# Kernel optimization log

Measured on AMD Instinct MI355X. Metric: run time of the kernel, lower is better.

The kernel has to match this reference:

```python
import jax, jax.numpy as jnp
import numpy as np

B, T, D, H = 4096, 512, 25, 25
NUM_LAYERS = 3


def setup_inputs() -> dict:
    key = jax.random.key(0)
    ks = jax.random.split(key, 9)
    s = 1.0 / np.sqrt(H)  # torch LSTM/Linear default init scale
    return {
        "x": jax.random.normal(ks[0], (B, T, D), dtype=jnp.float32),
        "Wih": jax.random.uniform(ks[1], (NUM_LAYERS, 4 * H, D), minval=-s, maxval=s),
        "Whh": jax.random.uniform(ks[2], (NUM_LAYERS, 4 * H, H), minval=-s, maxval=s),
        "bih": jax.random.uniform(ks[3], (NUM_LAYERS, 4 * H), minval=-s, maxval=s),
        "bhh": jax.random.uniform(ks[4], (NUM_LAYERS, 4 * H), minval=-s, maxval=s),
        "W1": jax.random.uniform(ks[5], (16, H), minval=-s, maxval=s),
        "b1": jax.random.uniform(ks[6], (16,), minval=-s, maxval=s),
        "W2": jax.random.uniform(ks[7], (14, 16), minval=-0.25, maxval=0.25),
        "b2": jax.random.uniform(ks[8], (14,), minval=-0.25, maxval=0.25),
    }


def _lstm_layer(x, Wih, Whh, b):
    """Single LSTM layer, batch_first. x: [B,T,Din] -> hs: [B,T,H].
    Torch gate order: i, f, g, o."""
    # Precompute input contribution for all timesteps at once: [B,T,4H]
    xg = jnp.einsum('btd,gd->btg', x, Wih) + b

    def step(carry, xg_t):
        h, c = carry
        g = xg_t + h @ Whh.T  # [B,4H]
        i, f, gg, o = jnp.split(g, 4, axis=-1)
        c = jax.nn.sigmoid(f) * c + jax.nn.sigmoid(i) * jnp.tanh(gg)
        h = jax.nn.sigmoid(o) * jnp.tanh(c)
        return (h, c), h

    h0 = jnp.zeros((x.shape[0], H), x.dtype)
    (_, _), hs = jax.lax.scan(step, (h0, h0), jnp.swapaxes(xg, 0, 1))  # [T,B,H]
    return jnp.swapaxes(hs, 0, 1)


def reference(x, Wih, Whh, bih, bhh, W1, b1, W2, b2):
    h = x
    for l in range(NUM_LAYERS):  # eval mode: inter-layer dropout disabled
        h = _lstm_layer(h, Wih[l], Whh[l], bih[l] + bhh[l])
    last = h[:, -1, :]                       # [B,H]
    out = jax.nn.relu(last @ W1.T + b1)      # [B,16]
    return jax.nn.softmax(out @ W2.T + b2, axis=1)  # [B,14]
```

## Files before the change

### kernel.cpp

```cpp
#include <hip/hip_runtime.h>


#define NBATCH 4096
#define NT     512
#define ND     25
#define NG     100
#define NL     3

__device__ __forceinline__ float sigf(float x) {
    return __builtin_amdgcn_rcpf(1.0f + __expf(-x));
}
__device__ __forceinline__ float tanhfast(float x) {
    float s = sigf(x + x);
    return s + s - 1.0f;
}

__global__ __launch_bounds__(256, 4)
void lstm2(const float* __restrict__ xin,
           const float* __restrict__ Wih,
           const float* __restrict__ Whh,
           const float* __restrict__ bih,
           const float* __restrict__ bhh,
           const float* __restrict__ W1,
           const float* __restrict__ b1,
           const float* __restrict__ W2,
           const float* __restrict__ b2,
           float* __restrict__ out,
           float* __restrict__ ws)
{
    __shared__ __align__(16) float xh[2][56];
    __shared__ float act[2][112];

    const int wid  = threadIdx.x >> 6;
    const int lane = threadIdx.x & 63;
    const int wb   = wid >> 1;
    const int role = wid & 1;
    const int b    = (blockIdx.x << 1) + wb;

    const int  lrow    = (lane < 50) ? lane : 49;
    const bool updater = (role == 0) && (lane < 25);

    float w[52];
    w[50] = 0.f; w[51] = 0.f;

    for (int l = 0; l < NL; ++l) {
        const int row = l * NG + role * 50 + lrow;
        const float* wihp = Wih + row * ND;
        const float* whhp = Whh + row * ND;
#pragma unroll
        for (int d = 0; d < 25; ++d) { w[d] = wihp[d]; w[25 + d] = whhp[d]; }
        const float bias = bih[row] + bhh[row];

        const float* src = (l == 0) ? (xin + (size_t)b * NT * ND)
                                    : (ws  + (size_t)b * NT * ND);
        float* wsrow = ws + (size_t)b * NT * ND;

        float c = 0.f;
        float xv_next = 0.f;
        if (updater) {
            xh[wb][lane] = src[lane];
            xv_next = src[ND + lane];
        }
        if (role == 0 && lane < 31) xh[wb][25 + lane] = 0.f;
        __syncthreads();

        for (int t = 0; t < NT; ++t) {
            float acc = bias;
#pragma unroll
            for (int c4 = 0; c4 < 13; ++c4) {
                const float4 v = *(const float4*)&xh[wb][c4 * 4];
                acc = fmaf(w[c4 * 4 + 0], v.x, acc);
                acc = fmaf(w[c4 * 4 + 1], v.y, acc);
                acc = fmaf(w[c4 * 4 + 2], v.z, acc);
                acc = fmaf(w[c4 * 4 + 3], v.w, acc);
            }
            float a;
            if (role == 0) a = sigf(acc);
            else           a = (lane < 25) ? tanhfast(acc)
                                           : sigf(acc);
            if (lane < 50) act[wb][role * 56 + lane] = a;
            __syncthreads();

            if (updater) {
                const float ig = act[wb][lane];
                const float fg = act[wb][25 + lane];
                const float gg = act[wb][56 + lane];
                const float og = act[wb][81 + lane];
                c = fmaf(fg, c, ig * gg);
                const float h = og * tanhfast(c);
                xh[wb][25 + lane] = h;
                xh[wb][lane]      = xv_next;
                if (l < 2) wsrow[t * ND + lane] = h;
                if (t + 2 < NT) xv_next = src[(t + 2) * ND + lane];
            }
            __syncthreads();
        }
    }

    if (role == 0 && lane < 16) {
        float u = b1[lane];
#pragma unroll
        for (int d = 0; d < 25; ++d) u = fmaf(W1[lane * 25 + d], xh[wb][25 + d], u);
        act[wb][lane] = fmaxf(u, 0.f);
    }
    if (role == 0 && lane < 14) {
        float lg = b2[lane];
#pragma unroll
        for (int r = 0; r < 16; ++r) lg = fmaf(W2[lane * 16 + r], act[wb][r], lg);
        act[wb][32 + lane] = lg;
    }
    if (role == 0 && lane < 14) {
        float m = -1e30f;
#pragma unroll
        for (int j = 0; j < 14; ++j) m = fmaxf(m, act[wb][32 + j]);
        float sum = 0.f;
#pragma unroll
        for (int j = 0; j < 14; ++j) sum += __expf(act[wb][32 + j] - m);
        out[b * 14 + lane] = __expf(act[wb][32 + lane] - m) / sum;
    }
}

extern "C" void kernel_launch(void* const* d_in, const int* in_sizes, int n_in,
                              void* d_out, int out_size, void* d_ws, size_t ws_size,
                              hipStream_t stream)
{
    const float* x   = (const float*)d_in[0];
    const float* Wih = (const float*)d_in[1];
    const float* Whh = (const float*)d_in[2];
    const float* bih = (const float*)d_in[3];
    const float* bhh = (const float*)d_in[4];
    const float* W1  = (const float*)d_in[5];
    const float* b1  = (const float*)d_in[6];
    const float* W2  = (const float*)d_in[7];
    const float* b2  = (const float*)d_in[8];
    float* outp = (float*)d_out;
    float* ws   = (float*)d_ws;

    dim3 grid(NBATCH / 2), block(256);
    hipLaunchKernelGGL(lstm2, grid, block, 0, stream,
                       x, Wih, Whh, bih, bhh, W1, b1, W2, b2, outp, ws);
}
```

Measured before the change: 1.884 ms.

## Rewrite LSTM recurrence as single-wave MFMA kernel with split-fp16 precision

Replaces the per-batch scalar FMA kernel, which used four waves per block with block-wide barriers each timestep, with one 64-thread wave per 16 batch rows. Gate pre-activations are computed with 16x16x32 fp16 MFMAs, using a hi/lo split of weights and inputs to approximate fp32 accuracy, and the bias is folded in through a constant-1 column. Each lane updates gates for its own rows in registers, so no workgroup barriers are needed, and inter-layer activations are stored as packed fp16 hi/lo pairs. The grid shrinks to 256 single-wave blocks, which may underuse the GPU's CUs, and the split-precision arithmetic introduces small numerical error.

```diff
diff --git a/kernel.cpp b/kernel.cpp
--- a/kernel.cpp
+++ b/kernel.cpp
@@ -1,22 +1,28 @@
 #include <hip/hip_runtime.h>
-
-
-#define NBATCH 4096
-#define NT     512
-#define ND     25
-#define NG     100
-#define NL     3
-
-__device__ __forceinline__ float sigf(float x) {
-    return __builtin_amdgcn_rcpf(1.0f + __expf(-x));
-}
-__device__ __forceinline__ float tanhfast(float x) {
-    float s = sigf(x + x);
-    return s + s - 1.0f;
-}
-
-__global__ __launch_bounds__(256, 4)
-void lstm2(const float* __restrict__ xin,
+#include <cstdint>
+
+
+typedef _Float16 f16;
+typedef f16  f16x8 __attribute__((ext_vector_type(8)));
+typedef float f32x4 __attribute__((ext_vector_type(4)));
+
+#define NT 512
+#define ND 25
+#define LOSCALE 4096.0f
+#define INVLO   2.44140625e-4f
+
+__device__ __forceinline__ float exp2f_(float x){ return __builtin_amdgcn_exp2f(x); }
+__device__ __forceinline__ float rcpf_(float x){ return __builtin_amdgcn_rcpf(x); }
+__device__ __forceinline__ float sigf(float x){ return rcpf_(1.f + exp2f_(-1.442695041f*x)); }
+__device__ __forceinline__ float tanhf_(float x){ return fmaf(2.f, rcpf_(1.f + exp2f_(-2.885390082f*x)), -1.f); }
+
+__device__ __forceinline__ unsigned short f16b(f16 h){ union{f16 h; unsigned short s;} u; u.h=h; return u.s; }
+__device__ __forceinline__ f16 b2f16(unsigned short s){ union{f16 h; unsigned short s;} u; u.s=s; return u.h; }
+
+#define MFMA(a,b,c) __builtin_amdgcn_mfma_f32_16x16x32_f16((a),(b),(c),0,0,0)
+
+__global__ __launch_bounds__(64, 1)
+void lstm9(const float* __restrict__ xin,
            const float* __restrict__ Wih,
            const float* __restrict__ Whh,
            const float* __restrict__ bih,
@@ -26,97 +32,206 @@
            const float* __restrict__ W2,
            const float* __restrict__ b2,
            float* __restrict__ out,
-           float* __restrict__ ws)
+           uint32_t* __restrict__ ws)
 {
-    __shared__ __align__(16) float xh[2][56];
-    __shared__ float act[2][112];
-
-    const int wid  = threadIdx.x >> 6;
-    const int lane = threadIdx.x & 63;
-    const int wb   = wid >> 1;
-    const int role = wid & 1;
-    const int b    = (blockIdx.x << 1) + wb;
-
-    const int  lrow    = (lane < 50) ? lane : 49;
-    const bool updater = (role == 0) && (lane < 25);
-
-    float w[52];
-    w[50] = 0.f; w[51] = 0.f;
-
-    for (int l = 0; l < NL; ++l) {
-        const int row = l * NG + role * 50 + lrow;
-        const float* wihp = Wih + row * ND;
-        const float* whhp = Whh + row * ND;
-#pragma unroll
-        for (int d = 0; d < 25; ++d) { w[d] = wihp[d]; w[25 + d] = whhp[d]; }
-        const float bias = bih[row] + bhh[row];
-
-        const float* src = (l == 0) ? (xin + (size_t)b * NT * ND)
-                                    : (ws  + (size_t)b * NT * ND);
-        float* wsrow = ws + (size_t)b * NT * ND;
-
-        float c = 0.f;
-        float xv_next = 0.f;
-        if (updater) {
-            xh[wb][lane] = src[lane];
-            xv_next = src[ND + lane];
-        }
-        if (role == 0 && lane < 31) xh[wb][25 + lane] = 0.f;
-        __syncthreads();
+    __shared__ __align__(16) f16 WH[14*64*8];
+    __shared__ __align__(16) f16 WL[14*64*8];
+    __shared__ __align__(16) f16 XH_H[16*72];
+    __shared__ __align__(16) f16 XH_L[16*72];
+    __shared__ __align__(16) float hfin[16*28];
+
+    const int L  = threadIdx.x;
+    const int bq = L & 15;
+    const int lg = L >> 4;
+    const int bb = blockIdx.x * 16;
+
+    for (int i = L; i < 16*72; i += 64) { XH_H[i] = (f16)0.f; XH_L[i] = (f16)0.f; }
+    if (L < 16) XH_H[L*72 + 63] = (f16)1.f;
+
+    float c0,c1,c2,c3,c4,c5,c6;
+    float h0=0,h1=0,h2=0,h3=0,h4=0,h5=0,h6=0;
+
+    for (int l = 0; l < 3; ++l) {
+        asm volatile("s_waitcnt vmcnt(0)" ::: "memory");
+
+        for (int blk = 0; blk < 14; ++blk) {
+            const int mt = blk >> 1, kt = blk & 1;
+            const int rp = mt*16 + bq;
+            const int u  = rp >> 2, g = rp & 3;
+            const int ro = g*25 + u;
+            f16x8 vh, vl;
+#pragma unroll
+            for (int i = 0; i < 8; ++i) {
+                const int k = kt*32 + lg*8 + i;
+                float w = 0.f;
+                if (rp < 100) {
+                    if (k < 25)       w = Wih[((size_t)l*100 + ro)*25 + k];
+                    else if (k < 50)  w = Whh[((size_t)l*100 + ro)*25 + (k-25)];
+                    else if (k == 63) w = bih[l*100 + ro] + bhh[l*100 + ro];
+                }
+                const f16 hi = (f16)w;
+                vh[i] = hi;
+                vl[i] = (f16)((w - (float)hi) * LOSCALE);
+            }
+            *(f16x8*)&WH[blk*512 + L*8] = vh;
+            *(f16x8*)&WL[blk*512 + L*8] = vl;
+        }
+
+        const bool isl0 = (l == 0);
+        const float*    srcx = xin + (size_t)(bb)*NT*ND;
+        const uint32_t* srcw = ws  + (size_t)(bb)*NT*ND;
+
+        c0=c1=c2=c3=c4=c5=c6=0.f;
+#pragma unroll
+        for (int j = 0; j < 7; ++j) {
+            const int u = lg + 4*j;
+            if (u < 25) {
+                XH_H[bq*72 + 25 + u] = (f16)0.f;
+                XH_L[bq*72 + 25 + u] = (f16)0.f;
+                f16 hi, lo;
+                if (isl0) {
+                    const float v = srcx[((size_t)bq*NT + 0)*ND + u];
+                    hi = (f16)v; lo = (f16)((v - (float)hi) * LOSCALE);
+                } else {
+                    const uint32_t p = srcw[((size_t)bq*NT + 0)*ND + u];
+                    hi = b2f16((unsigned short)(p & 0xffff));
+                    lo = b2f16((unsigned short)(p >> 16));
+                }
+                XH_H[bq*72 + u] = hi;
+                XH_L[bq*72 + u] = lo;
+            }
+        }
 
         for (int t = 0; t < NT; ++t) {
-            float acc = bias;
-#pragma unroll
-            for (int c4 = 0; c4 < 13; ++c4) {
-                const float4 v = *(const float4*)&xh[wb][c4 * 4];
-                acc = fmaf(w[c4 * 4 + 0], v.x, acc);
-                acc = fmaf(w[c4 * 4 + 1], v.y, acc);
-                acc = fmaf(w[c4 * 4 + 2], v.z, acc);
-                acc = fmaf(w[c4 * 4 + 3], v.w, acc);
-            }
-            float a;
-            if (role == 0) a = sigf(acc);
-            else           a = (lane < 25) ? tanhfast(acc)
-                                           : sigf(acc);
-            if (lane < 50) act[wb][role * 56 + lane] = a;
-            __syncthreads();
-
-            if (updater) {
-                const float ig = act[wb][lane];
-                const float fg = act[wb][25 + lane];
-                const float gg = act[wb][56 + lane];
-                const float og = act[wb][81 + lane];
-                c = fmaf(fg, c, ig * gg);
-                const float h = og * tanhfast(c);
-                xh[wb][25 + lane] = h;
-                xh[wb][lane]      = xv_next;
-                if (l < 2) wsrow[t * ND + lane] = h;
-                if (t + 2 < NT) xv_next = src[(t + 2) * ND + lane];
-            }
-            __syncthreads();
+            const f16x8 bh0 = *(const f16x8*)&XH_H[bq*72 +  0 + lg*8];
+            const f16x8 bh1 = *(const f16x8*)&XH_H[bq*72 + 32 + lg*8];
+            const f16x8 bl0 = *(const f16x8*)&XH_L[bq*72 +  0 + lg*8];
+            const f16x8 bl1 = *(const f16x8*)&XH_L[bq*72 + 32 + lg*8];
+
+            float    xnf0=0,xnf1=0,xnf2=0,xnf3=0,xnf4=0,xnf5=0,xnf6=0;
+            uint32_t xnp0=0,xnp1=0,xnp2=0,xnp3=0,xnp4=0,xnp5=0,xnp6=0;
+            if (t + 1 < NT) {
+#pragma unroll
+                for (int j = 0; j < 7; ++j) {
+                    const int u = lg + 4*j;
+                    if (u < 25) {
+                        if (isl0) {
+                            const float v = srcx[((size_t)bq*NT + (t+1))*ND + u];
+                            if (j==0) xnf0=v; else if (j==1) xnf1=v; else if (j==2) xnf2=v;
+                            else if (j==3) xnf3=v; else if (j==4) xnf4=v; else if (j==5) xnf5=v; else xnf6=v;
+                        } else {
+                            const uint32_t p = srcw[((size_t)bq*NT + (t+1))*ND + u];
+                            if (j==0) xnp0=p; else if (j==1) xnp1=p; else if (j==2) xnp2=p;
+                            else if (j==3) xnp3=p; else if (j==4) xnp4=p; else if (j==5) xnp5=p; else xnp6=p;
+                        }
+                    }
+                }
+            }
+
+            f32x4 d1_0={0,0,0,0},d1_1={0,0,0,0},d1_2={0,0,0,0},d1_3={0,0,0,0},
+                  d1_4={0,0,0,0},d1_5={0,0,0,0},d1_6={0,0,0,0};
+            f32x4 d2_0={0,0,0,0},d2_1={0,0,0,0},d2_2={0,0,0,0},d2_3={0,0,0,0},
+                  d2_4={0,0,0,0},d2_5={0,0,0,0},d2_6={0,0,0,0};
+#define DO_MT(mt, D1, D2)                                                     \
+            {                                                                  \
+                const f16x8 wh0 = *(const f16x8*)&WH[(mt*2+0)*512 + L*8];      \
+                const f16x8 wh1 = *(const f16x8*)&WH[(mt*2+1)*512 + L*8];      \
+                const f16x8 wl0 = *(const f16x8*)&WL[(mt*2+0)*512 + L*8];      \
+                const f16x8 wl1 = *(const f16x8*)&WL[(mt*2+1)*512 + L*8];      \
+                D1 = MFMA(wh0, bh0, D1);  D1 = MFMA(wh1, bh1, D1);             \
+                D2 = MFMA(wh0, bl0, D2);  D2 = MFMA(wh1, bl1, D2);             \
+                D2 = MFMA(wl0, bh0, D2);  D2 = MFMA(wl1, bh1, D2);             \
+            }
+            DO_MT(0, d1_0, d2_0) DO_MT(1, d1_1, d2_1) DO_MT(2, d1_2, d2_2)
+            DO_MT(3, d1_3, d2_3) DO_MT(4, d1_4, d2_4) DO_MT(5, d1_5, d2_5)
+            DO_MT(6, d1_6, d2_6)
+#undef DO_MT
+
+#define DO_UPD(D1, D2, C, H)                                                  \
+            {                                                                  \
+                const f32x4 dd = D1 + D2 * INVLO;                              \
+                const float gi = sigf(dd[0]);                                  \
+                const float gf = sigf(dd[1]);                                  \
+                const float gg = tanhf_(dd[2]);                                \
+                const float go = sigf(dd[3]);                                  \
+                C = fmaf(gf, C, gi * gg);                                      \
+                H = go * tanhf_(C);                                            \
+            }
+            DO_UPD(d1_0, d2_0, c0, h0) DO_UPD(d1_1, d2_1, c1, h1)
+            DO_UPD(d1_2, d2_2, c2, h2) DO_UPD(d1_3, d2_3, c3, h3)
+            DO_UPD(d1_4, d2_4, c4, h4) DO_UPD(d1_5, d2_5, c5, h5)
+            DO_UPD(d1_6, d2_6, c6, h6)
+#undef DO_UPD
+
+#pragma unroll
+            for (int j = 0; j < 7; ++j) {
+                const int u = 4*j + lg;
+                if (u < 25) {
+                    const float hv = (j==0)?h0:(j==1)?h1:(j==2)?h2:(j==3)?h3:(j==4)?h4:(j==5)?h5:h6;
+                    const f16 hi = (f16)hv;
+                    const f16 lo = (f16)((hv - (float)hi) * LOSCALE);
+                    XH_H[bq*72 + 25 + u] = hi;
+                    XH_L[bq*72 + 25 + u] = lo;
+                    if (l < 2) {
+                        const uint32_t p = (uint32_t)f16b(hi) | ((uint32_t)f16b(lo) << 16);
+                        ws[((size_t)(bb+bq)*NT + t)*ND + u] = p;
+                    }
+                }
+            }
+            if (t + 1 < NT) {
+#pragma unroll
+                for (int j = 0; j < 7; ++j) {
+                    const int u = lg + 4*j;
+                    if (u < 25) {
+                        f16 hi, lo;
+                        if (isl0) {
+                            const float v = (j==0)?xnf0:(j==1)?xnf1:(j==2)?xnf2:(j==3)?xnf3:(j==4)?xnf4:(j==5)?xnf5:xnf6;
+                            hi = (f16)v; lo = (f16)((v - (float)hi) * LOSCALE);
+                        } else {
+                            const uint32_t p = (j==0)?xnp0:(j==1)?xnp1:(j==2)?xnp2:(j==3)?xnp3:(j==4)?xnp4:(j==5)?xnp5:xnp6;
+                            hi = b2f16((unsigned short)(p & 0xffff));
+                            lo = b2f16((unsigned short)(p >> 16));
+                        }
+                        XH_H[bq*72 + u] = hi;
+                        XH_L[bq*72 + u] = lo;
+                    }
+                }
+            }
         }
     }
 
-    if (role == 0 && lane < 16) {
-        float u = b1[lane];
-#pragma unroll
-        for (int d = 0; d < 25; ++d) u = fmaf(W1[lane * 25 + d], xh[wb][25 + d], u);
-        act[wb][lane] = fmaxf(u, 0.f);
+#pragma unroll
+    for (int j = 0; j < 7; ++j) {
+        const int u = 4*j + lg;
+        if (u < 25) {
+            const float hv = (j==0)?h0:(j==1)?h1:(j==2)?h2:(j==3)?h3:(j==4)?h4:(j==5)?h5:h6;
+            hfin[bq*28 + u] = hv;
+        }
     }
-    if (role == 0 && lane < 14) {
-        float lg = b2[lane];
-#pragma unroll
-        for (int r = 0; r < 16; ++r) lg = fmaf(W2[lane * 16 + r], act[wb][r], lg);
-        act[wb][32 + lane] = lg;
-    }
-    if (role == 0 && lane < 14) {
-        float m = -1e30f;
-#pragma unroll
-        for (int j = 0; j < 14; ++j) m = fmaxf(m, act[wb][32 + j]);
-        float sum = 0.f;
-#pragma unroll
-        for (int j = 0; j < 14; ++j) sum += __expf(act[wb][32 + j] - m);
-        out[b * 14 + lane] = __expf(act[wb][32 + lane] - m) / sum;
+    if (L < 16) {
+        const int b = L;
+        float u1[16];
+#pragma unroll
+        for (int r = 0; r < 16; ++r) {
+            float acc = b1[r];
+#pragma unroll
+            for (int d = 0; d < 25; ++d) acc = fmaf(W1[r*25 + d], hfin[b*28 + d], acc);
+            u1[r] = fmaxf(acc, 0.f);
+        }
+        float lgt[14]; float m = -1e30f;
+#pragma unroll
+        for (int r = 0; r < 14; ++r) {
+            float acc = b2[r];
+#pragma unroll
+            for (int k = 0; k < 16; ++k) acc = fmaf(W2[r*16 + k], u1[k], acc);
+            lgt[r] = acc; m = fmaxf(m, acc);
+        }
+        float s = 0.f;
+#pragma unroll
+        for (int r = 0; r < 14; ++r) { lgt[r] = exp2f_(1.442695041f*(lgt[r]-m)); s += lgt[r]; }
+        const float inv = rcpf_(s);
+#pragma unroll
+        for (int r = 0; r < 14; ++r) out[(size_t)(bb+b)*14 + r] = lgt[r]*inv;
     }
 }
 
@@ -133,10 +248,10 @@
     const float* b1  = (const float*)d_in[6];
     const float* W2  = (const float*)d_in[7];
     const float* b2  = (const float*)d_in[8];
-    float* outp = (float*)d_out;
-    float* ws   = (float*)d_ws;
-
-    dim3 grid(NBATCH / 2), block(256);
-    hipLaunchKernelGGL(lstm2, grid, block, 0, stream,
+    float*    outp = (float*)d_out;
+    uint32_t* ws   = (uint32_t*)d_ws;
+
+    dim3 grid(4096 / 16), block(64);
+    hipLaunchKernelGGL(lstm9, grid, block, 0, stream,
                        x, Wih, Whh, bih, bhh, W1, b1, W2, b2, outp, ws);
 }
```

Result: slower. 2.986 ms (+58.5%).
